# Optimization experiments

Hardware: AMD Instinct MI355X
Metric: run time of the kernel (lower is better)

Reference implementation:

```python
import jax, jax.numpy as jnp
import numpy as np

D_MODEL = 1024
NUM_HEADS = 16
D_K = D_MODEL // NUM_HEADS
BATCH = 8
SEQ = 1024


def setup_inputs() -> dict:
    key = jax.random.key(0)
    ks = jax.random.split(key, 16)
    s = 1.0 / np.sqrt(D_MODEL)
    def lin(i):
        W = jax.random.uniform(ks[i], (D_MODEL, D_MODEL), jnp.float32, -s, s)
        b = jax.random.uniform(ks[i + 1], (D_MODEL,), jnp.float32, -s, s)
        return W, b
    Wq, bq = lin(0)
    Wk, bk = lin(2)
    Wv, bv = lin(4)
    Wg, bg = lin(6)
    Wbeta, bbeta = lin(8)
    Wo, bo = lin(10)
    X = jax.random.normal(ks[12], (BATCH, SEQ, D_MODEL), jnp.float32)
    Y = jax.random.normal(ks[13], (BATCH, SEQ, D_MODEL), jnp.float32)
    return dict(X=X, Y=Y, Wq=Wq, bq=bq, Wk=Wk, bk=bk, Wv=Wv, bv=bv,
                Wg=Wg, bg=bg, Wbeta=Wbeta, bbeta=bbeta, Wo=Wo, bo=bo)


def _split_heads(x):
    b, s, _ = x.shape
    return x.reshape(b, s, NUM_HEADS, D_K).transpose(0, 2, 1, 3)  # [b,h,s,d_k]


def _attend(q_in, kv_in, Wq, bq, Wk, bk, Wv, bv, Wg, bg, Wbeta, bbeta, Wo, bo):
    Q = _split_heads(q_in @ Wq + bq)
    K = _split_heads(kv_in @ Wk + bk)
    V = _split_heads(kv_in @ Wv + bv)
    scores = jnp.einsum('bhqd,bhkd->bhqk', Q, K) / jnp.sqrt(jnp.float32(D_K))
    attn = jax.nn.softmax(scores, axis=-1)
    ctx = jnp.einsum('bhqk,bhkd->bhqd', attn, V)
    b, h, s, d = ctx.shape
    ctx = ctx.transpose(0, 2, 1, 3).reshape(b, s, h * d)
    out = (ctx @ Wg + bg) * jnp.sqrt(jnp.float32(D_K)) + (ctx @ Wbeta + bbeta)
    return out @ Wo + bo


def reference(X, Y, Wq, bq, Wk, bk, Wv, bv, Wg, bg, Wbeta, bbeta, Wo, bo):
    params = (Wq, bq, Wk, bk, Wv, bv, Wg, bg, Wbeta, bbeta, Wo, bo)
    Y_new = _attend(X, Y, *params)   # pass 1: queries from X, keys/values from Y
    X_new = _attend(Y_new, X, *params)  # pass 2: queries from new Y, kv from original X
    return (X_new, Y_new)
```

## Files before the change

kernel.cpp:

```cpp
#include <hip/hip_runtime.h>

typedef unsigned short u16;
typedef __bf16 bf16x8 __attribute__((ext_vector_type(8)));
typedef float f32x4 __attribute__((ext_vector_type(4)));
typedef float f32x16 __attribute__((ext_vector_type(16)));
typedef u16 u16x4 __attribute__((ext_vector_type(4)));
typedef unsigned int u32x4v __attribute__((ext_vector_type(4)));

#define LOG2E_OVER_8 0.18033688011112043f

__device__ __forceinline__ u16 f2bf(float f) {
  union { float f; unsigned int u; } x{f};
  unsigned int r = (x.u + 0x7fffu + ((x.u >> 16) & 1u)) >> 16;
  return (u16)r;
}

__device__ __forceinline__ float bf2f(u16 v) {
  union { unsigned int u; float f; } x;
  x.u = ((unsigned int)v) << 16;
  return x.f;
}

__device__ __forceinline__ unsigned cvtpk(float a, float b) {
  unsigned r;
  asm("v_cvt_pk_bf16_f32 %0, %1, %2" : "=v"(r) : "v"(a), "v"(b));
  return r;
}

__device__ __forceinline__ void gld16(const void* g, void* l) {
  __builtin_amdgcn_global_load_lds((const __attribute__((address_space(1))) unsigned int*)g,
                                   (__attribute__((address_space(3))) unsigned int*)l,
                                   16, 0, 0);
}

__global__ void prep_w(const float* __restrict__ Wq, const float* __restrict__ Wk,
                       const float* __restrict__ Wv, const float* __restrict__ Wg,
                       const float* __restrict__ Wb, const float* __restrict__ Wo,
                       u16* __restrict__ Wqt, u16* __restrict__ Wkt, u16* __restrict__ Wvt,
                       u16* __restrict__ Wcn, u16* __restrict__ Wot)
{
  __shared__ float tile[32][33];
  const int m = blockIdx.z;
  const int nb = blockIdx.x * 32, kb = blockIdx.y * 32;
  const int tx = threadIdx.x, ty = threadIdx.y;
  const float* src = (m == 0) ? Wq : (m == 1) ? Wk : (m == 2) ? Wv : (m == 3) ? Wg : Wo;
  u16* dst = (m == 0) ? Wqt : (m == 1) ? Wkt : (m == 2) ? Wvt : (m == 3) ? Wcn : Wot;
#pragma unroll
  for (int i = 0; i < 4; ++i) {
    const int k = kb + ty + i * 8;
    float v = src[k * 1024 + nb + tx];
    if (m == 3) v = 8.0f * v + Wb[k * 1024 + nb + tx];
    if (m == 0) v *= LOG2E_OVER_8;
    if (m == 3) dst[k * 1024 + nb + tx] = f2bf(v);
    else        tile[ty + i * 8][tx] = v;
  }
  __syncthreads();
  if (m != 3) {
#pragma unroll
    for (int i = 0; i < 4; ++i) {
      const int r = ty + i * 8;
      dst[(nb + r) * 1024 + kb + tx] = f2bf(tile[tx][r]);
    }
  }
}

__global__ void prep_b(const float* __restrict__ bq, const float* __restrict__ bg,
                       const float* __restrict__ bb,
                       float* __restrict__ bqs, float* __restrict__ bcs)
{
  const int i = blockIdx.x * 256 + threadIdx.x;
  if (i < 1024) {
    bqs[i] = bq[i] * LOG2E_OVER_8;
    bcs[i] = 8.0f * bg[i] + bb[i];
  }
}

__global__ void bias_dot(const float* __restrict__ bcs, const u16* __restrict__ Wot,
                         const float* __restrict__ bo, float* __restrict__ bco)
{
  __shared__ float part[4];
  const int n = blockIdx.x, t = threadIdx.x;
  const u16* row = Wot + n * 1024;
  float a = 0.f;
#pragma unroll
  for (int i = 0; i < 4; ++i) {
    const int m = t + i * 256;
    a += bcs[m] * bf2f(row[m]);
  }
#pragma unroll
  for (int d = 1; d < 64; d <<= 1) a += __shfl_xor(a, d);
  if ((t & 63) == 0) part[t >> 6] = a;
  __syncthreads();
  if (t == 0) bco[n] = part[0] + part[1] + part[2] + part[3] + bo[n];
}

__global__ void cvt2_bf16(const float* __restrict__ in0, u16* __restrict__ out0,
                          const float* __restrict__ in1, u16* __restrict__ out1, int n)
{
  int i = (blockIdx.x * blockDim.x + threadIdx.x) * 4;
  const int stride = gridDim.x * blockDim.x * 4;
  for (; i < n; i += stride) {
    const float4 v0 = *reinterpret_cast<const float4*>(in0 + i);
    u16x4 o0;
    o0.x = f2bf(v0.x); o0.y = f2bf(v0.y); o0.z = f2bf(v0.z); o0.w = f2bf(v0.w);
    *reinterpret_cast<u16x4*>(out0 + i) = o0;
    const float4 v1 = *reinterpret_cast<const float4*>(in1 + i);
    u16x4 o1;
    o1.x = f2bf(v1.x); o1.y = f2bf(v1.y); o1.z = f2bf(v1.z); o1.w = f2bf(v1.w);
    *reinterpret_cast<u16x4*>(out1 + i) = o1;
  }
}

template<int EPI, int NB>
__device__ __forceinline__ void gemm_body(int bid0, u16* lA, u16* lB,
                                          const u16* __restrict__ A,
                                          const u16* __restrict__ Bt,
                                          const float* __restrict__ bias,
                                          u16* __restrict__ outb, float* __restrict__ outf)
{
  int bid = (bid0 & 7) * NB + (bid0 >> 3);
  const int row0 = (bid >> 3) * 128;
  const int col0 = (bid & 7) * 128;
  const int t = threadIdx.x;
  const int w = t >> 6, lane = t & 63;
  const int l15 = lane & 15, l4 = lane >> 4;
  const int wr = w >> 1, wc = w & 1;

  const int c0 = t, c1 = 256 + t;
  const u16* gA0 = A + (row0 + (c0 >> 2)) * 1024 + (c0 & 3) * 8;
  const u16* gA1 = A + (row0 + (c1 >> 2)) * 1024 + (c1 & 3) * 8;
  const u16* gB0 = Bt + (col0 + (c0 >> 2)) * 1024 + (c0 & 3) * 8;
  const u16* gB1 = Bt + (col0 + (c1 >> 2)) * 1024 + (c1 & 3) * 8;
  u16* lA0 = lA + (w * 64) * 8;
  u16* lA1 = lA + (256 + w * 64) * 8;
  u16* lB0 = lB + (w * 64) * 8;
  u16* lB1 = lB + (256 + w * 64) * 8;

  f32x4 acc[4][4] = {};

  for (int kt = 0; kt < 1024; kt += 32) {
    gld16(gA0 + kt, lA0);
    gld16(gA1 + kt, lA1);
    gld16(gB0 + kt, lB0);
    gld16(gB1 + kt, lB1);
    __syncthreads();
    bf16x8 aF[4], bF[4];
#pragma unroll
    for (int m = 0; m < 4; ++m)
      aF[m] = *reinterpret_cast<const bf16x8*>(&lA[(wr * 64 + m * 16 + l15) * 32 + l4 * 8]);
#pragma unroll
    for (int n = 0; n < 4; ++n)
      bF[n] = *reinterpret_cast<const bf16x8*>(&lB[(wc * 64 + n * 16 + l15) * 32 + l4 * 8]);
#pragma unroll
    for (int m = 0; m < 4; ++m)
#pragma unroll
      for (int n = 0; n < 4; ++n)
        acc[m][n] = __builtin_amdgcn_mfma_f32_16x16x32_bf16(aF[m], bF[n], acc[m][n], 0, 0, 0);
    __syncthreads();
  }

  float bv[4];
#pragma unroll
  for (int n = 0; n < 4; ++n)
    bv[n] = (EPI == 4) ? 0.0f : bias[col0 + wc * 64 + n * 16 + l15];
#pragma unroll
  for (int m = 0; m < 4; ++m) {
#pragma unroll
    for (int n = 0; n < 4; ++n) {
      const int c = col0 + wc * 64 + n * 16 + l15;
#pragma unroll
      for (int j = 0; j < 4; ++j) {
        const int r = row0 + wr * 64 + m * 16 + l4 * 4 + j;
        const float v = acc[m][n][j] + bv[n];
        if constexpr (EPI == 0 || EPI == 4) {
          outb[r * 1024 + c] = f2bf(v);
        } else if constexpr (EPI == 1) {
          outf[r * 1024 + c] = v;
          outb[r * 1024 + c] = f2bf(v);
        } else if constexpr (EPI == 2) {
          const int bi = r >> 10, s = r & 1023;
          const int h = c >> 6, d = c & 63;
          outb[((bi * 16 + h) * 64 + d) * 1024 + s] = f2bf(v);
        } else {
          outf[r * 1024 + c] = v;
        }
      }
    }
  }
}

template<int EPI, int NB = 64>
__global__ __launch_bounds__(256, 2)
void gemm_k(const u16* __restrict__ A, const u16* __restrict__ Bt,
            const float* __restrict__ bias,
            u16* __restrict__ outb, float* __restrict__ outf)
{
  __shared__ u16 lA[128 * 32];
  __shared__ u16 lB[128 * 32];
  gemm_body<EPI, NB>((int)blockIdx.x, lA, lB, A, Bt, bias, outb, outf);
}

__global__ __launch_bounds__(256, 2)
void gemm3_k(const u16* __restrict__ A0, const u16* __restrict__ B0,
             const float* __restrict__ c0, u16* __restrict__ o0,
             const u16* __restrict__ A1, const u16* __restrict__ B1,
             const float* __restrict__ c1, u16* __restrict__ o1,
             const u16* __restrict__ A2, const u16* __restrict__ B2,
             const float* __restrict__ c2, u16* __restrict__ o2,
             const u16* __restrict__ A3, const u16* __restrict__ B3,
             u16* __restrict__ o3)
{
  __shared__ u16 lA[128 * 32];
  __shared__ u16 lB[128 * 32];
  const int id = (int)blockIdx.x;
  if (id < 512)       gemm_body<0, 64>(id,        lA, lB, A0, B0, c0, o0, nullptr);
  else if (id < 1024) gemm_body<0, 64>(id - 512,  lA, lB, A1, B1, c1, o1, nullptr);
  else if (id < 1536) gemm_body<2, 64>(id - 1024, lA, lB, A2, B2, c2, o2, nullptr);
  else                gemm_body<4, 8>(id - 1536,  lA, lB, A3, B3, nullptr, o3, nullptr);
}

__global__ __launch_bounds__(256, 4)
void attn_k(const u16* __restrict__ Q, const u16* __restrict__ K,
            const u16* __restrict__ Vt, const u16* __restrict__ ctx_unused,
            u16* __restrict__ ctx)
{
  __shared__ u16 lK[64 * 72];
  __shared__ u16 lV[64 * 72];
  __shared__ float lsumI[4][32];
  const int id = (int)blockIdx.x;
  const int xcd = id & 7, o = id >> 3;
  const int pair = xcd * 16 + (o >> 3);
  const int qt = o & 7;
  const int b = pair >> 4, h = pair & 15;
  const int t = threadIdx.x, w = t >> 6, lane = t & 63;
  const int l31 = lane & 31, hi = lane >> 5;
  const int q0 = qt * 128 + w * 32;
  const u16* Qp = Q + (size_t)b * (1024 * 1024) + h * 64;
  const u16* Kp = K + (size_t)b * (1024 * 1024) + h * 64;
  const u16* Vp = Vt + (size_t)(b * 16 + h) * (64 * 1024);

  const int r0 = t >> 3, c0 = (t & 7) * 8;

  bf16x8 bQ[4];
#pragma unroll
  for (int ks = 0; ks < 4; ++ks)
    bQ[ks] = *reinterpret_cast<const bf16x8*>(&Qp[(q0 + l31) * 1024 + ks * 16 + hi * 8]);

  f32x16 acc[2] = {};
  float lsum = 0.f;

  bf16x8 sK0, sK1, sV0, sV1;
  sK0 = *reinterpret_cast<const bf16x8*>(&Kp[(r0) * 1024 + c0]);
  sK1 = *reinterpret_cast<const bf16x8*>(&Kp[(r0 + 32) * 1024 + c0]);
  sV0 = *reinterpret_cast<const bf16x8*>(&Vp[r0 * 1024 + c0]);
  sV1 = *reinterpret_cast<const bf16x8*>(&Vp[(r0 + 32) * 1024 + c0]);

  for (int it = 0; it < 16; ++it) {
    const int kv0 = it * 64;
    __syncthreads();
    *reinterpret_cast<bf16x8*>(&lK[r0 * 72 + c0]) = sK0;
    *reinterpret_cast<bf16x8*>(&lK[(r0 + 32) * 72 + c0]) = sK1;
    *reinterpret_cast<bf16x8*>(&lV[r0 * 72 + c0]) = sV0;
    *reinterpret_cast<bf16x8*>(&lV[(r0 + 32) * 72 + c0]) = sV1;
    __syncthreads();
    if (it + 1 < 16) {
      const int nk = kv0 + 64;
      sK0 = *reinterpret_cast<const bf16x8*>(&Kp[(nk + r0) * 1024 + c0]);
      sK1 = *reinterpret_cast<const bf16x8*>(&Kp[(nk + r0 + 32) * 1024 + c0]);
      sV0 = *reinterpret_cast<const bf16x8*>(&Vp[r0 * 1024 + nk + c0]);
      sV1 = *reinterpret_cast<const bf16x8*>(&Vp[(r0 + 32) * 1024 + nk + c0]);
    }

    f32x16 sS[2] = {};
    __builtin_amdgcn_s_setprio(1);
#pragma unroll
    for (int tt = 0; tt < 2; ++tt) {
#pragma unroll
      for (int ks = 0; ks < 4; ++ks) {
        const bf16x8 aK = *reinterpret_cast<const bf16x8*>(
            &lK[(tt * 32 + l31) * 72 + ks * 16 + hi * 8]);
        sS[tt] = __builtin_amdgcn_mfma_f32_32x32x16_bf16(aK, bQ[ks], sS[tt], 0, 0, 0);
      }
    }
    __builtin_amdgcn_s_setprio(0);

    unsigned pa[2][2][4];
#pragma unroll
    for (int tt = 0; tt < 2; ++tt) {
      float p[16];
      float s0 = 0.f, s1 = 0.f, s2 = 0.f, s3 = 0.f;
#pragma unroll
      for (int r = 0; r < 16; r += 4) {
        p[r]     = __builtin_amdgcn_exp2f(sS[tt][r]);
        p[r + 1] = __builtin_amdgcn_exp2f(sS[tt][r + 1]);
        p[r + 2] = __builtin_amdgcn_exp2f(sS[tt][r + 2]);
        p[r + 3] = __builtin_amdgcn_exp2f(sS[tt][r + 3]);
        s0 += p[r]; s1 += p[r + 1]; s2 += p[r + 2]; s3 += p[r + 3];
      }
      lsum += (s0 + s1) + (s2 + s3);
      unsigned wv[8];
#pragma unroll
      for (int i = 0; i < 8; ++i) wv[i] = cvtpk(p[2 * i], p[2 * i + 1]);
#pragma unroll
      for (int c = 0; c < 2; ++c) {
        const unsigned pw0 = (unsigned)__shfl_xor((int)wv[4 * c + 0], 32);
        const unsigned pw1 = (unsigned)__shfl_xor((int)wv[4 * c + 1], 32);
        const unsigned pw2 = (unsigned)__shfl_xor((int)wv[4 * c + 2], 32);
        const unsigned pw3 = (unsigned)__shfl_xor((int)wv[4 * c + 3], 32);
        pa[tt][c][0] = hi ? pw2 : wv[4 * c + 0];
        pa[tt][c][1] = hi ? pw3 : wv[4 * c + 1];
        pa[tt][c][2] = hi ? wv[4 * c + 2] : pw0;
        pa[tt][c][3] = hi ? wv[4 * c + 3] : pw1;
      }
    }

    __builtin_amdgcn_s_setprio(1);
#pragma unroll
    for (int tt = 0; tt < 2; ++tt)
#pragma unroll
      for (int c = 0; c < 2; ++c) {
        u32x4v pw;
        pw.x = pa[tt][c][0]; pw.y = pa[tt][c][1];
        pw.z = pa[tt][c][2]; pw.w = pa[tt][c][3];
        const bf16x8 aP = __builtin_bit_cast(bf16x8, pw);
#pragma unroll
        for (int dt = 0; dt < 2; ++dt) {
          const bf16x8 bV = *reinterpret_cast<const bf16x8*>(
              &lV[(dt * 32 + l31) * 72 + tt * 32 + c * 16 + hi * 8]);
          acc[dt] = __builtin_amdgcn_mfma_f32_32x32x16_bf16(aP, bV, acc[dt], 0, 0, 0);
        }
      }
    __builtin_amdgcn_s_setprio(0);
  }

  const float ltot = lsum + __shfl_xor(lsum, 32);
  if (hi == 0) lsumI[w][l31] = 1.0f / ltot;
  u16* Cp = ctx + (size_t)b * (1024 * 1024) + h * 64;
#pragma unroll
  for (int dt = 0; dt < 2; ++dt)
#pragma unroll
    for (int r = 0; r < 16; ++r) {
      const int q = (r & 3) + 8 * (r >> 2) + 4 * hi;
      const float inv = lsumI[w][q];
      Cp[(q0 + q) * 1024 + dt * 32 + l31] = f2bf(acc[dt][r] * inv);
    }
}

extern "C" void kernel_launch(void* const* d_in, const int* in_sizes, int n_in,
                              void* d_out, int out_size, void* d_ws, size_t ws_size,
                              hipStream_t stream)
{
  (void)in_sizes; (void)n_in; (void)out_size; (void)ws_size;
  const float* X  = (const float*)d_in[0];
  const float* Y  = (const float*)d_in[1];
  const float* Wq = (const float*)d_in[2];
  const float* bq = (const float*)d_in[3];
  const float* Wk = (const float*)d_in[4];
  const float* bk = (const float*)d_in[5];
  const float* Wv = (const float*)d_in[6];
  const float* bv = (const float*)d_in[7];
  const float* Wg = (const float*)d_in[8];
  const float* bg = (const float*)d_in[9];
  const float* Wb = (const float*)d_in[10];
  const float* bb = (const float*)d_in[11];
  const float* Wo = (const float*)d_in[12];
  const float* bo = (const float*)d_in[13];
  float* out = (float*)d_out;
  char* ws = (char*)d_ws;
  const size_t MB = 1024ull * 1024ull;

  u16* Wqt = (u16*)(ws + 0 * MB);
  u16* Wkt = (u16*)(ws + 2 * MB);
  u16* Wvt = (u16*)(ws + 4 * MB);
  u16* Wcn = (u16*)(ws + 6 * MB);
  u16* Wot = (u16*)(ws + 8 * MB);
  u16* Wcot = (u16*)(ws + 10 * MB);
  u16* Xb = (u16*)(ws + 12 * MB);
  u16* Yb = (u16*)(ws + 28 * MB);
  u16* Qb = (u16*)(ws + 44 * MB);
  u16* Kb = (u16*)(ws + 60 * MB);
  u16* Vt = (u16*)(ws + 76 * MB);
  u16* Cx = (u16*)(ws + 92 * MB);
  float* bqs = (float*)(ws + 108 * MB);
  float* bcs = (float*)(ws + 108 * MB + 4096);
  float* bco = (float*)(ws + 108 * MB + 8192);
  const int NEL = 8 * 1024 * 1024;

  prep_w<<<dim3(32, 32, 5), dim3(32, 8), 0, stream>>>(Wq, Wk, Wv, Wg, Wb, Wo,
                                                      Wqt, Wkt, Wvt, Wcn, Wot);
  prep_b<<<4, 256, 0, stream>>>(bq, bg, bb, bqs, bcs);
  bias_dot<<<1024, 256, 0, stream>>>(bcs, Wot, bo, bco);
  cvt2_bf16<<<2048, 256, 0, stream>>>(X, Xb, Y, Yb, NEL);

  gemm3_k<<<1600, 256, 0, stream>>>(Xb, Wqt, bqs, Qb,
                                    Yb, Wkt, bk, Kb,
                                    Yb, Wvt, bv, Vt,
                                    Wot, Wcn, Wcot);
  attn_k<<<dim3(1024), 256, 0, stream>>>(Qb, Kb, Vt, nullptr, Cx);
  gemm_k<1><<<512, 256, 0, stream>>>(Cx, Wcot, bco, Yb, out + NEL);

  gemm3_k<<<1536, 256, 0, stream>>>(Yb, Wqt, bqs, Qb,
                                    Xb, Wkt, bk, Kb,
                                    Xb, Wvt, bv, Vt,
                                    nullptr, nullptr, nullptr);
  attn_k<<<dim3(1024), 256, 0, stream>>>(Qb, Kb, Vt, nullptr, Cx);
  gemm_k<3><<<512, 256, 0, stream>>>(Cx, Wcot, bco, nullptr, out);
}
```

Measured before the change: 322.9 us.

## Double GEMM K-tile to 64 with XOR-swizzled LDS and fold bias_dot into gemm3

The GEMM main loop now stages 64-wide K slices per iteration instead of 32. This halves the number of barrier pairs and issues two MFMAs per fragment pair. LDS rows are XOR-swizzled in 16-byte chunks so the wider fragment reads avoid bank conflicts. The separate bias_dot launch is removed and its work is appended as extra blocks of the first gemm3 launch, with one wavefront per output column. In exchange, LDS use per block doubles (32 KB), which may limit occupancy.

```diff
diff --git a/kernel.cpp b/kernel.cpp
--- a/kernel.cpp
+++ b/kernel.cpp
@@ -73,25 +73,6 @@
     bqs[i] = bq[i] * LOG2E_OVER_8;
     bcs[i] = 8.0f * bg[i] + bb[i];
   }
-}
-
-__global__ void bias_dot(const float* __restrict__ bcs, const u16* __restrict__ Wot,
-                         const float* __restrict__ bo, float* __restrict__ bco)
-{
-  __shared__ float part[4];
-  const int n = blockIdx.x, t = threadIdx.x;
-  const u16* row = Wot + n * 1024;
-  float a = 0.f;
-#pragma unroll
-  for (int i = 0; i < 4; ++i) {
-    const int m = t + i * 256;
-    a += bcs[m] * bf2f(row[m]);
-  }
-#pragma unroll
-  for (int d = 1; d < 64; d <<= 1) a += __shfl_xor(a, d);
-  if ((t & 63) == 0) part[t >> 6] = a;
-  __syncthreads();
-  if (t == 0) bco[n] = part[0] + part[1] + part[2] + part[3] + bo[n];
 }
 
 __global__ void cvt2_bf16(const float* __restrict__ in0, u16* __restrict__ out0,
@@ -125,37 +106,48 @@
   const int w = t >> 6, lane = t & 63;
   const int l15 = lane & 15, l4 = lane >> 4;
   const int wr = w >> 1, wc = w & 1;
-
-  const int c0 = t, c1 = 256 + t;
-  const u16* gA0 = A + (row0 + (c0 >> 2)) * 1024 + (c0 & 3) * 8;
-  const u16* gA1 = A + (row0 + (c1 >> 2)) * 1024 + (c1 & 3) * 8;
-  const u16* gB0 = Bt + (col0 + (c0 >> 2)) * 1024 + (c0 & 3) * 8;
-  const u16* gB1 = Bt + (col0 + (c1 >> 2)) * 1024 + (c1 & 3) * 8;
-  u16* lA0 = lA + (w * 64) * 8;
-  u16* lA1 = lA + (256 + w * 64) * 8;
-  u16* lB0 = lB + (w * 64) * 8;
-  u16* lB1 = lB + (256 + w * 64) * 8;
+  const int l7 = l15 & 7;
+
+  const u16* gA[4];
+  const u16* gB[4];
+#pragma unroll
+  for (int k2 = 0; k2 < 4; ++k2) {
+    const int c = k2 * 256 + t;
+    const int r = c >> 3;
+    const int sc = ((c & 7) ^ (r & 7)) * 8;
+    gA[k2] = A + (row0 + r) * 1024 + sc;
+    gB[k2] = Bt + (col0 + r) * 1024 + sc;
+  }
 
   f32x4 acc[4][4] = {};
 
-  for (int kt = 0; kt < 1024; kt += 32) {
-    gld16(gA0 + kt, lA0);
-    gld16(gA1 + kt, lA1);
-    gld16(gB0 + kt, lB0);
-    gld16(gB1 + kt, lB1);
+  for (int kt = 0; kt < 1024; kt += 64) {
+#pragma unroll
+    for (int k2 = 0; k2 < 4; ++k2) {
+      gld16(gA[k2] + kt, lA + (k2 * 256 + w * 64) * 8);
+      gld16(gB[k2] + kt, lB + (k2 * 256 + w * 64) * 8);
+    }
     __syncthreads();
-    bf16x8 aF[4], bF[4];
+    bf16x8 aF[4][2], bF[4][2];
 #pragma unroll
     for (int m = 0; m < 4; ++m)
-      aF[m] = *reinterpret_cast<const bf16x8*>(&lA[(wr * 64 + m * 16 + l15) * 32 + l4 * 8]);
+#pragma unroll
+      for (int ks = 0; ks < 2; ++ks)
+        aF[m][ks] = *reinterpret_cast<const bf16x8*>(
+            &lA[(wr * 64 + m * 16 + l15) * 64 + ((ks * 4 + l4) ^ l7) * 8]);
 #pragma unroll
     for (int n = 0; n < 4; ++n)
-      bF[n] = *reinterpret_cast<const bf16x8*>(&lB[(wc * 64 + n * 16 + l15) * 32 + l4 * 8]);
+#pragma unroll
+      for (int ks = 0; ks < 2; ++ks)
+        bF[n][ks] = *reinterpret_cast<const bf16x8*>(
+            &lB[(wc * 64 + n * 16 + l15) * 64 + ((ks * 4 + l4) ^ l7) * 8]);
 #pragma unroll
     for (int m = 0; m < 4; ++m)
 #pragma unroll
-      for (int n = 0; n < 4; ++n)
-        acc[m][n] = __builtin_amdgcn_mfma_f32_16x16x32_bf16(aF[m], bF[n], acc[m][n], 0, 0, 0);
+      for (int n = 0; n < 4; ++n) {
+        acc[m][n] = __builtin_amdgcn_mfma_f32_16x16x32_bf16(aF[m][0], bF[n][0], acc[m][n], 0, 0, 0);
+        acc[m][n] = __builtin_amdgcn_mfma_f32_16x16x32_bf16(aF[m][1], bF[n][1], acc[m][n], 0, 0, 0);
+      }
     __syncthreads();
   }
 
@@ -189,14 +181,30 @@
   }
 }
 
+__device__ __forceinline__ void bias_body(int bb, const float* __restrict__ bcs,
+                                          const u16* __restrict__ Wot,
+                                          const float* __restrict__ bo,
+                                          float* __restrict__ bco)
+{
+  const int t = threadIdx.x, w = t >> 6, l = t & 63;
+  const int n = bb * 4 + w;
+  const u16* row = Wot + n * 1024;
+  float a = 0.f;
+#pragma unroll
+  for (int i = 0; i < 16; ++i) a += bcs[l + 64 * i] * bf2f(row[l + 64 * i]);
+#pragma unroll
+  for (int d = 1; d < 64; d <<= 1) a += __shfl_xor(a, d);
+  if (l == 0) bco[n] = a + bo[n];
+}
+
 template<int EPI, int NB = 64>
 __global__ __launch_bounds__(256, 2)
 void gemm_k(const u16* __restrict__ A, const u16* __restrict__ Bt,
             const float* __restrict__ bias,
             u16* __restrict__ outb, float* __restrict__ outf)
 {
-  __shared__ u16 lA[128 * 32];
-  __shared__ u16 lB[128 * 32];
+  __shared__ u16 lA[128 * 64];
+  __shared__ u16 lB[128 * 64];
   gemm_body<EPI, NB>((int)blockIdx.x, lA, lB, A, Bt, bias, outb, outf);
 }
 
@@ -208,15 +216,18 @@
              const u16* __restrict__ A2, const u16* __restrict__ B2,
              const float* __restrict__ c2, u16* __restrict__ o2,
              const u16* __restrict__ A3, const u16* __restrict__ B3,
-             u16* __restrict__ o3)
-{
-  __shared__ u16 lA[128 * 32];
-  __shared__ u16 lB[128 * 32];
+             u16* __restrict__ o3,
+             const float* __restrict__ bcs, const float* __restrict__ bo,
+             float* __restrict__ bco)
+{
+  __shared__ u16 lA[128 * 64];
+  __shared__ u16 lB[128 * 64];
   const int id = (int)blockIdx.x;
   if (id < 512)       gemm_body<0, 64>(id,        lA, lB, A0, B0, c0, o0, nullptr);
   else if (id < 1024) gemm_body<0, 64>(id - 512,  lA, lB, A1, B1, c1, o1, nullptr);
   else if (id < 1536) gemm_body<2, 64>(id - 1024, lA, lB, A2, B2, c2, o2, nullptr);
-  else                gemm_body<4, 8>(id - 1536,  lA, lB, A3, B3, nullptr, o3, nullptr);
+  else if (id < 1600) gemm_body<4, 8>(id - 1536,  lA, lB, A3, B3, nullptr, o3, nullptr);
+  else                bias_body(id - 1600, bcs, A3, bo, bco);
 }
 
 __global__ __launch_bounds__(256, 4)
@@ -389,19 +400,20 @@
   prep_w<<<dim3(32, 32, 5), dim3(32, 8), 0, stream>>>(Wq, Wk, Wv, Wg, Wb, Wo,
                                                       Wqt, Wkt, Wvt, Wcn, Wot);
   prep_b<<<4, 256, 0, stream>>>(bq, bg, bb, bqs, bcs);
-  bias_dot<<<1024, 256, 0, stream>>>(bcs, Wot, bo, bco);
   cvt2_bf16<<<2048, 256, 0, stream>>>(X, Xb, Y, Yb, NEL);
 
-  gemm3_k<<<1600, 256, 0, stream>>>(Xb, Wqt, bqs, Qb,
+  gemm3_k<<<1856, 256, 0, stream>>>(Xb, Wqt, bqs, Qb,
                                     Yb, Wkt, bk, Kb,
                                     Yb, Wvt, bv, Vt,
-                                    Wot, Wcn, Wcot);
+                                    Wot, Wcn, Wcot,
+                                    bcs, bo, bco);
   attn_k<<<dim3(1024), 256, 0, stream>>>(Qb, Kb, Vt, nullptr, Cx);
   gemm_k<1><<<512, 256, 0, stream>>>(Cx, Wcot, bco, Yb, out + NEL);
 
   gemm3_k<<<1536, 256, 0, stream>>>(Yb, Wqt, bqs, Qb,
                                     Xb, Wkt, bk, Kb,
                                     Xb, Wvt, bv, Vt,
+                                    nullptr, nullptr, nullptr,
                                     nullptr, nullptr, nullptr);
   attn_k<<<dim3(1024), 256, 0, stream>>>(Qb, Kb, Vt, nullptr, Cx);
   gemm_k<3><<<512, 256, 0, stream>>>(Cx, Wcot, bco, nullptr, out);
```

Result: faster. 286.3 us (-11.3%).
